# Kernel optimization log

Hardware: AMD Instinct MI355X
Metric: run time of the kernel (lower is better)

## Reference

```python
import jax, jax.numpy as jnp
import numpy as np
import math

B, S, E, H = 2, 4096, 1024, 1024

def setup_inputs() -> dict:
    key = jax.random.key(0)
    ks = jax.random.split(key, 7)
    X = jax.random.normal(ks[0], (B, S, E), dtype=jnp.float32)
    attention_mask = jnp.ones((B, S, S), dtype=jnp.int32)
    sc = 1.0 / math.sqrt(E)
    Wq = jax.random.normal(ks[1], (H, E), dtype=jnp.float32) * sc
    Wk = jax.random.normal(ks[2], (H, E), dtype=jnp.float32) * sc
    Wv = jax.random.normal(ks[3], (H, E), dtype=jnp.float32) * sc
    bq = jnp.zeros((H,), dtype=jnp.float32)
    bk = jnp.zeros((H,), dtype=jnp.float32)
    bv = jnp.zeros((H,), dtype=jnp.float32)
    return {"X": X, "attention_mask": attention_mask,
            "Wq": Wq, "bq": bq, "Wk": Wk, "bk": bk, "Wv": Wv, "bv": bv}

def reference(X, attention_mask, Wq, bq, Wk, bk, Wv, bv):
    # Linear layers: y = x @ W^T + b (torch convention W is [out, in])
    Q = jnp.einsum('bse,he->bsh', X, Wq) + bq
    K = jnp.einsum('bse,he->bsh', X, Wk) + bk
    V = jnp.einsum('bse,he->bsh', X, Wv) + bv
    scale = 1.0 / math.sqrt(H)
    scores = jnp.einsum('bqh,bkh->bqk', Q, K) * scale  # [B,S,S]
    scores = jnp.where(attention_mask == 0, -jnp.inf, scores)
    # dropout (eval mode -> identity) would be applied here, BEFORE softmax
    weights = jax.nn.softmax(scores, axis=-1)
    out = jnp.einsum('bqk,bkh->bqh', weights, V)  # [B,S,H]
    return out
```

## Files before the change

kernel.cpp:

```cpp
#include <hip/hip_runtime.h>
#include <stdint.h>


typedef __bf16 bf16;
typedef __attribute__((ext_vector_type(4))) __bf16 bf16x4;
typedef __attribute__((ext_vector_type(8))) __bf16 bf16x8;
typedef __attribute__((ext_vector_type(4))) float f32x4;

__device__ __forceinline__ void g2l16(const void* g, void* l) {
  __builtin_amdgcn_global_load_lds(
      (const __attribute__((address_space(1))) uint32_t*)g,
      (__attribute__((address_space(3))) uint32_t*)l, 16, 0, 0);
}

__device__ __forceinline__ f32x4 ds_read128(uint32_t addr) {
  f32x4 d;
  asm volatile("ds_read_b128 %0, %1" : "=v"(d) : "v"(addr));
  return d;
}

template <int V> struct IC { static constexpr int value = V; };
template <bool V> struct BC { static constexpr bool value = V; };

template <int N> __device__ __forceinline__ void waitvm() {
  if constexpr (N == 6) asm volatile("s_waitcnt vmcnt(6)" ::: "memory");
  else if constexpr (N == 4) asm volatile("s_waitcnt vmcnt(4)" ::: "memory");
  else if constexpr (N == 0) asm volatile("s_waitcnt vmcnt(0)" ::: "memory");
}

__global__ __launch_bounds__(256) void cvt_all(
    const float* __restrict__ X, const float* __restrict__ Wq,
    const float* __restrict__ Wk, const float* __restrict__ Wv,
    bf16* __restrict__ X_bf, bf16* __restrict__ W_bf) {
  const int bid = blockIdx.x;
  const float* src;
  bf16* dst;
  int i;
  if (bid < 4096) {
    i = (bid * 256 + threadIdx.x) * 8;
    src = X; dst = X_bf;
  } else {
    i = ((bid - 4096) * 256 + threadIdx.x) * 8;
    const int seg = i >> 20;
    const int off = i & 1048575;
    src = (seg == 0) ? Wq : (seg == 1) ? Wk : Wv;
    dst = W_bf;
    f32x4 a = *(const f32x4*)(src + off);
    f32x4 b = *(const f32x4*)(src + off + 4);
    bf16x8 o;
#pragma unroll
    for (int e = 0; e < 4; ++e) { o[e] = (bf16)a[e]; o[4 + e] = (bf16)b[e]; }
    *(bf16x8*)(dst + i) = o;
    return;
  }
  f32x4 a = *(const f32x4*)(src + i);
  f32x4 b = *(const f32x4*)(src + i + 4);
  bf16x8 o;
#pragma unroll
  for (int e = 0; e < 4; ++e) { o[e] = (bf16)a[e]; o[4 + e] = (bf16)b[e]; }
  *(bf16x8*)(dst + i) = o;
}

template <int NT>
__device__ __forceinline__ void kloop256(
    const bf16* __restrict__ Ag, const bf16* __restrict__ Bg, const int KA,
    const int KB, bf16* lds, f32x4 (&acc)[8][4]) {
  const int tid = threadIdx.x;
  const int lane = tid & 63;
  const int wave = tid >> 6;
  const int l15 = lane & 15, quad = lane >> 4;
  const int wrow = (wave >> 2) * 128;
  const int wcol = (wave & 3) * 64;
  const int srow = tid >> 3;
  const int scol = ((tid & 7) ^ (srow & 7)) * 8;
  const int swz = l15 & 7;

  const uint32_t lds_u = (uint32_t)(uintptr_t)lds;
  const uint32_t a_l15 = lds_u + (uint32_t)((wrow + l15) * 128);
  const uint32_t b_l15 = lds_u + 32768u + (uint32_t)((wcol + l15) * 128);
  const uint32_t ck0 = (uint32_t)(((quad) ^ swz) * 16);
  const uint32_t ck1 = (uint32_t)(((4 + quad) ^ swz) * 16);

  auto stg = [&](int t, int h) {
    bf16* base = lds + (t & 1) * 32768;
    if (h == 0) {
      const bf16* g = Bg + (size_t)srow * KB + t * 64 + scol;
      g2l16(g, base + 16384 + tid * 8);
      g2l16(g + (size_t)64 * KB, base + 16384 + tid * 8 + 4096);
    } else if (h == 1) {
      const bf16* g = Bg + (size_t)(128 + srow) * KB + t * 64 + scol;
      g2l16(g, base + 24576 + tid * 8);
      g2l16(g + (size_t)64 * KB, base + 24576 + tid * 8 + 4096);
    } else if (h == 2) {
      const bf16* g = Ag + (size_t)srow * KA + t * 64 + scol;
      g2l16(g, base + tid * 8);
      g2l16(g + (size_t)128 * KA, base + tid * 8 + 8192);
    } else {
      const bf16* g = Ag + (size_t)(64 + srow) * KA + t * 64 + scol;
      g2l16(g, base + 4096 + tid * 8);
      g2l16(g + (size_t)128 * KA, base + 4096 + tid * 8 + 8192);
    }
  };

  f32x4 brf[2][4];
  auto phase = [&](int t, auto qc, int st, int sh, auto dsc, auto vmc) {
    constexpr int q = decltype(qc)::value;
    constexpr bool ds = decltype(dsc)::value;
    constexpr int vm = decltype(vmc)::value;
    const uint32_t bb = (t & 1) ? 65536u : 0u;
    f32x4 ar[2][2];
#pragma unroll
    for (int i = 0; i < 2; ++i) {
      ar[i][0] = ds_read128(a_l15 + bb + (uint32_t)((2 * q + i) * 2048) + ck0);
      ar[i][1] = ds_read128(a_l15 + bb + (uint32_t)((2 * q + i) * 2048) + ck1);
    }
    if constexpr (q == 0) {
#pragma unroll
      for (int j = 0; j < 4; ++j) {
        brf[0][j] = ds_read128(b_l15 + bb + (uint32_t)(j * 2048) + ck0);
        brf[1][j] = ds_read128(b_l15 + bb + (uint32_t)(j * 2048) + ck1);
      }
    }
    if constexpr (ds) stg(st, sh);
    __builtin_amdgcn_s_barrier();
    asm volatile("s_waitcnt lgkmcnt(0)" ::: "memory");
    __builtin_amdgcn_sched_barrier(0);
    __builtin_amdgcn_s_setprio(1);
#pragma unroll
    for (int ks = 0; ks < 2; ++ks)
#pragma unroll
      for (int i = 0; i < 2; ++i)
#pragma unroll
        for (int j = 0; j < 4; ++j)
          acc[2 * q + i][j] = __builtin_amdgcn_mfma_f32_16x16x32_bf16(
              __builtin_bit_cast(bf16x8, ar[i][ks]),
              __builtin_bit_cast(bf16x8, brf[ks][j]),
              acc[2 * q + i][j], 0, 0, 0);
    __builtin_amdgcn_s_setprio(0);
    waitvm<vm>();
    __builtin_amdgcn_s_barrier();
  };

  stg(0, 0); stg(0, 1); stg(0, 2); stg(0, 3);
  stg(1, 0); stg(1, 1); stg(1, 2);
  asm volatile("s_waitcnt vmcnt(6)" ::: "memory");
  __builtin_amdgcn_s_barrier();

  constexpr int NI = NT / 2;
#pragma unroll 1
  for (int u = 0; u < NI - 1; ++u) {
    const int t0 = 2 * u, t1 = t0 + 1;
    phase(t0, IC<0>{}, t1, 3, BC<true>{}, IC<-1>{});
    phase(t0, IC<1>{}, t0 + 2, 0, BC<true>{}, IC<-1>{});
    phase(t0, IC<2>{}, t0 + 2, 1, BC<true>{}, IC<-1>{});
    phase(t0, IC<3>{}, t0 + 2, 2, BC<true>{}, IC<6>{});
    phase(t1, IC<0>{}, t0 + 2, 3, BC<true>{}, IC<-1>{});
    phase(t1, IC<1>{}, t0 + 3, 0, BC<true>{}, IC<-1>{});
    phase(t1, IC<2>{}, t0 + 3, 1, BC<true>{}, IC<-1>{});
    phase(t1, IC<3>{}, t0 + 3, 2, BC<true>{}, IC<6>{});
  }
  {
    const int t0 = NT - 2, t1 = NT - 1;
    phase(t0, IC<0>{}, t1, 3, BC<true>{}, IC<-1>{});
    phase(t0, IC<1>{}, 0, 0, BC<false>{}, IC<-1>{});
    phase(t0, IC<2>{}, 0, 0, BC<false>{}, IC<-1>{});
    phase(t0, IC<3>{}, 0, 0, BC<false>{}, IC<0>{});
    phase(t1, IC<0>{}, 0, 0, BC<false>{}, IC<-1>{});
    phase(t1, IC<1>{}, 0, 0, BC<false>{}, IC<-1>{});
    phase(t1, IC<2>{}, 0, 0, BC<false>{}, IC<-1>{});
    phase(t1, IC<3>{}, 0, 0, BC<false>{}, IC<-1>{});
  }
}

__global__ __launch_bounds__(256, 2) void gemm_qkv(
    const bf16* __restrict__ Xb, const bf16* __restrict__ Wb3,
    const float* __restrict__ bq, const float* __restrict__ bk,
    const float* __restrict__ bv, bf16* __restrict__ QK,
    bf16* __restrict__ Vt)
{
  constexpr int K = 1024, N = 1024;
  __shared__ __align__(16) bf16 ldsA[128 * 64];
  __shared__ __align__(16) bf16 ldsB[128 * 64];

  const int tid  = threadIdx.x;
  const int lane = tid & 63;
  const int wave = tid >> 6;
  const int d = blockIdx.y * 64 + blockIdx.x;
  const int xcd = d & 7, slot = d >> 3;
  const int g = xcd * 8 + slot / 24;
  const int c = slot % 24;
  const int which = c >> 3;
  const int n0 = (c & 7) * 128;
  const int m0 = g * 128;
  const bf16* Bt = Wb3 + (size_t)which * 1048576;
  const float* bias = (which == 0) ? bq : ((which == 1) ? bk : bv);

  const int l15  = lane & 15;
  const int quad = lane >> 4;
  const int wm = (wave >> 1) * 64;
  const int wn = (wave & 1) * 64;
  const int sw = l15 & 7;

  f32x4 acc[4][4];
#pragma unroll
  for (int i = 0; i < 4; ++i)
#pragma unroll
    for (int j = 0; j < 4; ++j) acc[i][j] = f32x4{0.f, 0.f, 0.f, 0.f};

  const int srow = tid >> 3;
  const int scol = ((tid & 7) ^ (srow & 7)) * 8;
  const size_t a_base = (size_t)(m0 + srow) * K + scol;
  const size_t b_base = (size_t)(n0 + srow) * K + scol;
  const int lds_off = tid * 8;

  for (int kt = 0; kt < K; kt += 64) {
    const bf16* ga = Xb + a_base + kt;
    const bf16* gb = Bt + b_base + kt;
#pragma unroll
    for (int it = 0; it < 4; ++it) {
      g2l16(ga + (size_t)(it * 32) * K, &ldsA[lds_off + it * 2048]);
      g2l16(gb + (size_t)(it * 32) * K, &ldsB[lds_off + it * 2048]);
    }
    __syncthreads();
#pragma unroll
    for (int ks = 0; ks < 2; ++ks) {
      const int ch = ks * 4 + quad;
      bf16x8 af[4], bfg[4];
#pragma unroll
      for (int i = 0; i < 4; ++i)
        af[i] = *(const bf16x8*)&ldsA[(wm + i * 16 + l15) * 64 + (ch ^ sw) * 8];
#pragma unroll
      for (int j = 0; j < 4; ++j)
        bfg[j] = *(const bf16x8*)&ldsB[(wn + j * 16 + l15) * 64 + (ch ^ sw) * 8];
#pragma unroll
      for (int i = 0; i < 4; ++i)
#pragma unroll
        for (int j = 0; j < 4; ++j)
          acc[i][j] = __builtin_amdgcn_mfma_f32_16x16x32_bf16(
              af[i], bfg[j], acc[i][j], 0, 0, 0);
    }
    __syncthreads();
  }

  if (which < 2) {
    bf16* C = QK + (size_t)which * (size_t)(8192 * 1024);
#pragma unroll
    for (int i = 0; i < 4; ++i) {
#pragma unroll
      for (int j = 0; j < 4; ++j) {
        const int r = m0 + wm + i * 16 + quad * 4;
        const int cc = n0 + wn + j * 16 + l15;
        const float bvv = bias[cc];
        f32x4 v = acc[i][j];
#pragma unroll
        for (int reg = 0; reg < 4; ++reg)
          C[(size_t)(r + reg) * N + cc] = (bf16)(v[reg] + bvv);
      }
    }
  } else {
#pragma unroll
    for (int i = 0; i < 4; ++i) {
#pragma unroll
      for (int j = 0; j < 4; ++j) {
        const int r = m0 + wm + i * 16 + quad * 4;
        const int cc = n0 + wn + j * 16 + l15;
        const int b = r >> 12, s = r & 4095;
        const float bvv = bias[cc];
        f32x4 v = acc[i][j];
        bf16x4 o;
#pragma unroll
        for (int reg = 0; reg < 4; ++reg) o[reg] = (bf16)(v[reg] + bvv);
        *(bf16x4*)&Vt[((size_t)(b * 1024 + cc)) * 4096 + s] = o;
      }
    }
  }
}

__global__ __launch_bounds__(512, 2) void gemm_scores(
    const bf16* __restrict__ Q, const bf16* __restrict__ Kb,
    const int* __restrict__ mask, bf16* __restrict__ P,
    float* __restrict__ psum) {
  __shared__ __align__(16) bf16 lds[2 * 32768];
  const int bid = blockIdx.y * 32 + blockIdx.x;
  const int sb = (bid & 7) * 64 + (bid >> 3);
  const int bx = sb & 31, by = sb >> 5;
  const int m0 = bx * 256;
  const int n0 = by * 256;
  const int batch = m0 >> 12;
  const bf16* Ag = Q + (size_t)m0 * 1024;
  const bf16* Bg = Kb + (size_t)batch * (size_t)(4096 * 1024) +
                   (size_t)n0 * 1024;

  f32x4 acc[8][4];
#pragma unroll
  for (int i = 0; i < 8; ++i)
#pragma unroll
    for (int j = 0; j < 4; ++j) acc[i][j] = f32x4{0.f, 0.f, 0.f, 0.f};

  kloop256<16>(Ag, Bg, 1024, 1024, lds, acc);

  const int lane = threadIdx.x & 63, wave = threadIdx.x >> 6;
  const int l15 = lane & 15, quad = lane >> 4;
  const int wrow = (wave >> 2) * 128, wcol = (wave & 3) * 64;
  float* ps = psum + (size_t)(by * 4 + (wave & 3)) * 8192;

#pragma unroll
  for (int i = 0; i < 8; ++i) {
    const int r = m0 + wrow + i * 16 + quad * 4;
    f32x4 rsum = f32x4{0.f, 0.f, 0.f, 0.f};
#pragma unroll
    for (int j = 0; j < 4; ++j) {
      const int c = n0 + wcol + j * 16 + l15;
      f32x4 v = acc[i][j];
#pragma unroll
      for (int reg = 0; reg < 4; ++reg) {
        float e = __expf(v[reg] * 0.03125f);
        if (mask[(size_t)(r + reg) * 4096 + c] == 0) e = 0.f;
        P[(size_t)(r + reg) * 4096 + c] = (bf16)e;
        rsum[reg] += e;
      }
    }
#pragma unroll
    for (int off = 1; off < 16; off <<= 1) {
#pragma unroll
      for (int reg = 0; reg < 4; ++reg)
        rsum[reg] += __shfl_xor(rsum[reg], off);
    }
    if (l15 == 0) {
#pragma unroll
      for (int reg = 0; reg < 4; ++reg) ps[r + reg] = rsum[reg];
    }
  }
}

__global__ __launch_bounds__(256, 2) void gemm_pv(
    const bf16* __restrict__ A, const bf16* __restrict__ Bt,
    const float* __restrict__ psum, float* __restrict__ C)
{
  constexpr int N = 1024, K = 4096;
  __shared__ __align__(16) bf16 ldsA[128 * 64];
  __shared__ __align__(16) bf16 ldsB[128 * 64];

  const int tid  = threadIdx.x;
  const int lane = tid & 63;
  const int wave = tid >> 6;
  const int d = blockIdx.y * 64 + blockIdx.x;
  const int xcd = d & 7, slot = d >> 3;
  const int g = xcd * 8 + (slot >> 3);
  const int h = slot & 7;
  const int m0 = g * 128;
  const int n0 = h * 128;
  const int batch = m0 >> 12;
  const bf16* Btb = Bt + (size_t)batch * (size_t)(1024 * 4096);

  const int l15  = lane & 15;
  const int quad = lane >> 4;
  const int wm = (wave >> 1) * 64;
  const int wn = (wave & 1) * 64;
  const int sw = l15 & 7;

  f32x4 acc[4][4];
#pragma unroll
  for (int i = 0; i < 4; ++i)
#pragma unroll
    for (int j = 0; j < 4; ++j) acc[i][j] = f32x4{0.f, 0.f, 0.f, 0.f};

  const int srow = tid >> 3;
  const int scol = ((tid & 7) ^ (srow & 7)) * 8;
  const size_t a_base = (size_t)(m0 + srow) * K + scol;
  const size_t b_base = (size_t)(n0 + srow) * K + scol;
  const int lds_off = tid * 8;

  for (int kt = 0; kt < K; kt += 64) {
    const bf16* ga = A + a_base + kt;
    const bf16* gb = Btb + b_base + kt;
#pragma unroll
    for (int it = 0; it < 4; ++it) {
      g2l16(ga + (size_t)(it * 32) * K, &ldsA[lds_off + it * 2048]);
      g2l16(gb + (size_t)(it * 32) * K, &ldsB[lds_off + it * 2048]);
    }
    __syncthreads();
#pragma unroll
    for (int ks = 0; ks < 2; ++ks) {
      const int ch = ks * 4 + quad;
      bf16x8 af[4], bfg[4];
#pragma unroll
      for (int i = 0; i < 4; ++i)
        af[i] = *(const bf16x8*)&ldsA[(wm + i * 16 + l15) * 64 + (ch ^ sw) * 8];
#pragma unroll
      for (int j = 0; j < 4; ++j)
        bfg[j] = *(const bf16x8*)&ldsB[(wn + j * 16 + l15) * 64 + (ch ^ sw) * 8];
#pragma unroll
      for (int i = 0; i < 4; ++i)
#pragma unroll
        for (int j = 0; j < 4; ++j)
          acc[i][j] = __builtin_amdgcn_mfma_f32_16x16x32_bf16(
              af[i], bfg[j], acc[i][j], 0, 0, 0);
    }
    __syncthreads();
  }

  float* linv = (float*)ldsA;
  if (tid < 128) {
    float s = 0.f;
#pragma unroll 8
    for (int p = 0; p < 64; ++p) s += psum[(size_t)p * 8192 + m0 + tid];
    linv[tid] = 1.0f / s;
  }
  __syncthreads();

#pragma unroll
  for (int i = 0; i < 4; ++i) {
    const int lr = wm + i * 16 + quad * 4;
    const int r = m0 + lr;
    f32x4 inv;
#pragma unroll
    for (int reg = 0; reg < 4; ++reg) inv[reg] = linv[lr + reg];
#pragma unroll
    for (int j = 0; j < 4; ++j) {
      const int c = n0 + wn + j * 16 + l15;
      f32x4 v = acc[i][j];
#pragma unroll
      for (int reg = 0; reg < 4; ++reg)
        C[(size_t)(r + reg) * N + c] = v[reg] * inv[reg];
    }
  }
}

extern "C" void kernel_launch(void* const* d_in, const int* in_sizes, int n_in,
                              void* d_out, int out_size, void* d_ws,
                              size_t ws_size, hipStream_t stream) {
  const float* X   = (const float*)d_in[0];
  const int* mask  = (const int*)d_in[1];
  const float* Wq  = (const float*)d_in[2];
  const float* bq  = (const float*)d_in[3];
  const float* Wk  = (const float*)d_in[4];
  const float* bk  = (const float*)d_in[5];
  const float* Wv  = (const float*)d_in[6];
  const float* bv  = (const float*)d_in[7];
  float* out = (float*)d_out;

  const size_t QKV_ELEMS = (size_t)8192 * 1024;
  bf16* Q    = (bf16*)d_ws;
  bf16* Kb   = Q + QKV_ELEMS;
  bf16* X_bf = Kb + QKV_ELEMS;
  bf16* Vt   = X_bf + QKV_ELEMS;
  bf16* Sc   = Vt + QKV_ELEMS;
  bf16* W_bf = Sc;
  float* psum = (float*)X_bf;

  cvt_all<<<dim3(5632), dim3(256), 0, stream>>>(X, Wq, Wk, Wv, X_bf, W_bf);
  gemm_qkv<<<dim3(64, 24), dim3(256), 0, stream>>>(X_bf, W_bf, bq, bk, bv, Q,
                                                   Vt);
  gemm_scores<<<dim3(32, 16), dim3(512), 0, stream>>>(Q, Kb, mask, Sc, psum);
  gemm_pv<<<dim3(64, 8), dim3(256), 0, stream>>>(Sc, Vt, psum, out);
}
```

Before: 414.6 us.

## Switch all GEMM kernels from 16x16x32 to 32x32x16 MFMA tiles

Replaces the 16x16x32 bf16 MFMA instruction with 32x32x16 across the QKV projection, QK^T/softmax and PV kernels. Fragment loading, LDS addressing, accumulator layout and epilogue index mapping are reworked for the 32x32 output layout. The larger MFMA tile needs fewer LDS reads per FLOP and fewer instructions, which should lift matrix-core throughput. In exchange the epilogue stores are more scattered, and the row-sum reduction needs wider shuffles over 16 registers each.

```diff
diff --git a/kernel.cpp b/kernel.cpp
--- a/kernel.cpp
+++ b/kernel.cpp
@@ -6,6 +6,7 @@
 typedef __attribute__((ext_vector_type(4))) __bf16 bf16x4;
 typedef __attribute__((ext_vector_type(8))) __bf16 bf16x8;
 typedef __attribute__((ext_vector_type(4))) float f32x4;
+typedef __attribute__((ext_vector_type(16))) float f32x16;
 
 __device__ __forceinline__ void g2l16(const void* g, void* l) {
   __builtin_amdgcn_global_load_lds(
@@ -64,22 +65,24 @@
 template <int NT>
 __device__ __forceinline__ void kloop256(
     const bf16* __restrict__ Ag, const bf16* __restrict__ Bg, const int KA,
-    const int KB, bf16* lds, f32x4 (&acc)[8][4]) {
+    const int KB, bf16* lds, f32x16 (&acc)[4][2]) {
   const int tid = threadIdx.x;
   const int lane = tid & 63;
   const int wave = tid >> 6;
-  const int l15 = lane & 15, quad = lane >> 4;
+  const int l31 = lane & 31, hi = lane >> 5;
   const int wrow = (wave >> 2) * 128;
   const int wcol = (wave & 3) * 64;
   const int srow = tid >> 3;
   const int scol = ((tid & 7) ^ (srow & 7)) * 8;
-  const int swz = l15 & 7;
+  const int swz = l31 & 7;
 
   const uint32_t lds_u = (uint32_t)(uintptr_t)lds;
-  const uint32_t a_l15 = lds_u + (uint32_t)((wrow + l15) * 128);
-  const uint32_t b_l15 = lds_u + 32768u + (uint32_t)((wcol + l15) * 128);
-  const uint32_t ck0 = (uint32_t)(((quad) ^ swz) * 16);
-  const uint32_t ck1 = (uint32_t)(((4 + quad) ^ swz) * 16);
+  const uint32_t a_l = lds_u + (uint32_t)((wrow + l31) * 128);
+  const uint32_t b_l = lds_u + 32768u + (uint32_t)((wcol + l31) * 128);
+  uint32_t ckk[4];
+#pragma unroll
+  for (int ks = 0; ks < 4; ++ks)
+    ckk[ks] = (uint32_t)(((ks * 2 + hi) ^ swz) * 16);
 
   auto stg = [&](int t, int h) {
     bf16* base = lds + (t & 1) * 32768;
@@ -108,18 +111,16 @@
     constexpr bool ds = decltype(dsc)::value;
     constexpr int vm = decltype(vmc)::value;
     const uint32_t bb = (t & 1) ? 65536u : 0u;
-    f32x4 ar[2][2];
-#pragma unroll
-    for (int i = 0; i < 2; ++i) {
-      ar[i][0] = ds_read128(a_l15 + bb + (uint32_t)((2 * q + i) * 2048) + ck0);
-      ar[i][1] = ds_read128(a_l15 + bb + (uint32_t)((2 * q + i) * 2048) + ck1);
-    }
+    f32x4 ar[4];
+#pragma unroll
+    for (int ks = 0; ks < 4; ++ks)
+      ar[ks] = ds_read128(a_l + bb + (uint32_t)(q * 4096) + ckk[ks]);
     if constexpr (q == 0) {
 #pragma unroll
-      for (int j = 0; j < 4; ++j) {
-        brf[0][j] = ds_read128(b_l15 + bb + (uint32_t)(j * 2048) + ck0);
-        brf[1][j] = ds_read128(b_l15 + bb + (uint32_t)(j * 2048) + ck1);
-      }
+      for (int nj = 0; nj < 2; ++nj)
+#pragma unroll
+        for (int ks = 0; ks < 4; ++ks)
+          brf[nj][ks] = ds_read128(b_l + bb + (uint32_t)(nj * 4096) + ckk[ks]);
     }
     if constexpr (ds) stg(st, sh);
     __builtin_amdgcn_s_barrier();
@@ -127,15 +128,13 @@
     __builtin_amdgcn_sched_barrier(0);
     __builtin_amdgcn_s_setprio(1);
 #pragma unroll
-    for (int ks = 0; ks < 2; ++ks)
-#pragma unroll
-      for (int i = 0; i < 2; ++i)
-#pragma unroll
-        for (int j = 0; j < 4; ++j)
-          acc[2 * q + i][j] = __builtin_amdgcn_mfma_f32_16x16x32_bf16(
-              __builtin_bit_cast(bf16x8, ar[i][ks]),
-              __builtin_bit_cast(bf16x8, brf[ks][j]),
-              acc[2 * q + i][j], 0, 0, 0);
+    for (int ks = 0; ks < 4; ++ks)
+#pragma unroll
+      for (int nj = 0; nj < 2; ++nj)
+        acc[q][nj] = __builtin_amdgcn_mfma_f32_32x32x16_bf16(
+            __builtin_bit_cast(bf16x8, ar[ks]),
+            __builtin_bit_cast(bf16x8, brf[nj][ks]),
+            acc[q][nj], 0, 0, 0);
     __builtin_amdgcn_s_setprio(0);
     waitvm<vm>();
     __builtin_amdgcn_s_barrier();
@@ -188,24 +187,23 @@
   const int d = blockIdx.y * 64 + blockIdx.x;
   const int xcd = d & 7, slot = d >> 3;
   const int g = xcd * 8 + slot / 24;
-  const int c = slot % 24;
-  const int which = c >> 3;
-  const int n0 = (c & 7) * 128;
+  const int c3 = slot % 24;
+  const int which = c3 >> 3;
+  const int n0 = (c3 & 7) * 128;
   const int m0 = g * 128;
   const bf16* Bt = Wb3 + (size_t)which * 1048576;
   const float* bias = (which == 0) ? bq : ((which == 1) ? bk : bv);
 
-  const int l15  = lane & 15;
-  const int quad = lane >> 4;
+  const int l31 = lane & 31, hi = lane >> 5;
   const int wm = (wave >> 1) * 64;
   const int wn = (wave & 1) * 64;
-  const int sw = l15 & 7;
-
-  f32x4 acc[4][4];
-#pragma unroll
-  for (int i = 0; i < 4; ++i)
-#pragma unroll
-    for (int j = 0; j < 4; ++j) acc[i][j] = f32x4{0.f, 0.f, 0.f, 0.f};
+  const int sw = l31 & 7;
+
+  f32x16 acc[2][2];
+#pragma unroll
+  for (int i = 0; i < 2; ++i)
+#pragma unroll
+    for (int j = 0; j < 2; ++j) acc[i][j] = (f32x16)(0.f);
 
   const int srow = tid >> 3;
   const int scol = ((tid & 7) ^ (srow & 7)) * 8;
@@ -223,21 +221,21 @@
     }
     __syncthreads();
 #pragma unroll
-    for (int ks = 0; ks < 2; ++ks) {
-      const int ch = ks * 4 + quad;
-      bf16x8 af[4], bfg[4];
-#pragma unroll
-      for (int i = 0; i < 4; ++i)
-        af[i] = *(const bf16x8*)&ldsA[(wm + i * 16 + l15) * 64 + (ch ^ sw) * 8];
-#pragma unroll
-      for (int j = 0; j < 4; ++j)
-        bfg[j] = *(const bf16x8*)&ldsB[(wn + j * 16 + l15) * 64 + (ch ^ sw) * 8];
-#pragma unroll
-      for (int i = 0; i < 4; ++i)
-#pragma unroll
-        for (int j = 0; j < 4; ++j)
-          acc[i][j] = __builtin_amdgcn_mfma_f32_16x16x32_bf16(
-              af[i], bfg[j], acc[i][j], 0, 0, 0);
+    for (int ks = 0; ks < 4; ++ks) {
+      const int ch = (ks * 2 + hi) ^ sw;
+      bf16x8 af[2], bfg[2];
+#pragma unroll
+      for (int mi = 0; mi < 2; ++mi)
+        af[mi] = *(const bf16x8*)&ldsA[(wm + mi * 32 + l31) * 64 + ch * 8];
+#pragma unroll
+      for (int nj = 0; nj < 2; ++nj)
+        bfg[nj] = *(const bf16x8*)&ldsB[(wn + nj * 32 + l31) * 64 + ch * 8];
+#pragma unroll
+      for (int mi = 0; mi < 2; ++mi)
+#pragma unroll
+        for (int nj = 0; nj < 2; ++nj)
+          acc[mi][nj] = __builtin_amdgcn_mfma_f32_32x32x16_bf16(
+              af[mi], bfg[nj], acc[mi][nj], 0, 0, 0);
     }
     __syncthreads();
   }
@@ -245,32 +243,37 @@
   if (which < 2) {
     bf16* C = QK + (size_t)which * (size_t)(8192 * 1024);
 #pragma unroll
-    for (int i = 0; i < 4; ++i) {
-#pragma unroll
-      for (int j = 0; j < 4; ++j) {
-        const int r = m0 + wm + i * 16 + quad * 4;
-        const int cc = n0 + wn + j * 16 + l15;
+    for (int mi = 0; mi < 2; ++mi) {
+      const int rb = m0 + wm + mi * 32 + 4 * hi;
+#pragma unroll
+      for (int nj = 0; nj < 2; ++nj) {
+        const int cc = n0 + wn + nj * 32 + l31;
         const float bvv = bias[cc];
-        f32x4 v = acc[i][j];
-#pragma unroll
-        for (int reg = 0; reg < 4; ++reg)
-          C[(size_t)(r + reg) * N + cc] = (bf16)(v[reg] + bvv);
+#pragma unroll
+        for (int gq = 0; gq < 4; ++gq)
+#pragma unroll
+          for (int k = 0; k < 4; ++k)
+            C[(size_t)(rb + 8 * gq + k) * N + cc] =
+                (bf16)(acc[mi][nj][4 * gq + k] + bvv);
       }
     }
   } else {
 #pragma unroll
-    for (int i = 0; i < 4; ++i) {
-#pragma unroll
-      for (int j = 0; j < 4; ++j) {
-        const int r = m0 + wm + i * 16 + quad * 4;
-        const int cc = n0 + wn + j * 16 + l15;
-        const int b = r >> 12, s = r & 4095;
+    for (int mi = 0; mi < 2; ++mi) {
+      const int rb = m0 + wm + mi * 32 + 4 * hi;
+#pragma unroll
+      for (int nj = 0; nj < 2; ++nj) {
+        const int cc = n0 + wn + nj * 32 + l31;
         const float bvv = bias[cc];
-        f32x4 v = acc[i][j];
-        bf16x4 o;
-#pragma unroll
-        for (int reg = 0; reg < 4; ++reg) o[reg] = (bf16)(v[reg] + bvv);
-        *(bf16x4*)&Vt[((size_t)(b * 1024 + cc)) * 4096 + s] = o;
+#pragma unroll
+        for (int gq = 0; gq < 4; ++gq) {
+          const int r0 = rb + 8 * gq;
+          const int b = r0 >> 12, s = r0 & 4095;
+          bf16x4 o;
+#pragma unroll
+          for (int k = 0; k < 4; ++k) o[k] = (bf16)(acc[mi][nj][4 * gq + k] + bvv);
+          *(bf16x4*)&Vt[((size_t)(b * 1024 + cc)) * 4096 + s] = o;
+        }
       }
     }
   }
@@ -291,44 +294,47 @@
   const bf16* Bg = Kb + (size_t)batch * (size_t)(4096 * 1024) +
                    (size_t)n0 * 1024;
 
-  f32x4 acc[8][4];
-#pragma unroll
-  for (int i = 0; i < 8; ++i)
-#pragma unroll
-    for (int j = 0; j < 4; ++j) acc[i][j] = f32x4{0.f, 0.f, 0.f, 0.f};
+  f32x16 acc[4][2];
+#pragma unroll
+  for (int i = 0; i < 4; ++i)
+#pragma unroll
+    for (int j = 0; j < 2; ++j) acc[i][j] = (f32x16)(0.f);
 
   kloop256<16>(Ag, Bg, 1024, 1024, lds, acc);
 
   const int lane = threadIdx.x & 63, wave = threadIdx.x >> 6;
-  const int l15 = lane & 15, quad = lane >> 4;
+  const int l31 = lane & 31, hi = lane >> 5;
   const int wrow = (wave >> 2) * 128, wcol = (wave & 3) * 64;
   float* ps = psum + (size_t)(by * 4 + (wave & 3)) * 8192;
 
 #pragma unroll
-  for (int i = 0; i < 8; ++i) {
-    const int r = m0 + wrow + i * 16 + quad * 4;
-    f32x4 rsum = f32x4{0.f, 0.f, 0.f, 0.f};
-#pragma unroll
-    for (int j = 0; j < 4; ++j) {
-      const int c = n0 + wcol + j * 16 + l15;
-      f32x4 v = acc[i][j];
-#pragma unroll
-      for (int reg = 0; reg < 4; ++reg) {
-        float e = __expf(v[reg] * 0.03125f);
-        if (mask[(size_t)(r + reg) * 4096 + c] == 0) e = 0.f;
-        P[(size_t)(r + reg) * 4096 + c] = (bf16)e;
+  for (int mi = 0; mi < 4; ++mi) {
+    const int rb = m0 + wrow + mi * 32 + 4 * hi;
+    float rsum[16];
+#pragma unroll
+    for (int reg = 0; reg < 16; ++reg) rsum[reg] = 0.f;
+#pragma unroll
+    for (int nj = 0; nj < 2; ++nj) {
+      const int c = n0 + wcol + nj * 32 + l31;
+#pragma unroll
+      for (int reg = 0; reg < 16; ++reg) {
+        const int r = rb + (reg & 3) + 8 * (reg >> 2);
+        float e = __expf(acc[mi][nj][reg] * 0.03125f);
+        if (mask[(size_t)r * 4096 + c] == 0) e = 0.f;
+        P[(size_t)r * 4096 + c] = (bf16)e;
         rsum[reg] += e;
       }
     }
 #pragma unroll
-    for (int off = 1; off < 16; off <<= 1) {
-#pragma unroll
-      for (int reg = 0; reg < 4; ++reg)
+    for (int off = 1; off < 32; off <<= 1) {
+#pragma unroll
+      for (int reg = 0; reg < 16; ++reg)
         rsum[reg] += __shfl_xor(rsum[reg], off);
     }
-    if (l15 == 0) {
-#pragma unroll
-      for (int reg = 0; reg < 4; ++reg) ps[r + reg] = rsum[reg];
+    if (l31 == 0) {
+#pragma unroll
+      for (int reg = 0; reg < 16; ++reg)
+        ps[rb + (reg & 3) + 8 * (reg >> 2)] = rsum[reg];
     }
   }
 }
@@ -353,17 +359,16 @@
   const int batch = m0 >> 12;
   const bf16* Btb = Bt + (size_t)batch * (size_t)(1024 * 4096);
 
-  const int l15  = lane & 15;
-  const int quad = lane >> 4;
+  const int l31 = lane & 31, hi = lane >> 5;
   const int wm = (wave >> 1) * 64;
   const int wn = (wave & 1) * 64;
-  const int sw = l15 & 7;
-
-  f32x4 acc[4][4];
-#pragma unroll
-  for (int i = 0; i < 4; ++i)
-#pragma unroll
-    for (int j = 0; j < 4; ++j) acc[i][j] = f32x4{0.f, 0.f, 0.f, 0.f};
+  const int sw = l31 & 7;
+
+  f32x16 acc[2][2];
+#pragma unroll
+  for (int i = 0; i < 2; ++i)
+#pragma unroll
+    for (int j = 0; j < 2; ++j) acc[i][j] = (f32x16)(0.f);
 
   const int srow = tid >> 3;
   const int scol = ((tid & 7) ^ (srow & 7)) * 8;
@@ -381,21 +386,21 @@
     }
     __syncthreads();
 #pragma unroll
-    for (int ks = 0; ks < 2; ++ks) {
-      const int ch = ks * 4 + quad;
-      bf16x8 af[4], bfg[4];
-#pragma unroll
-      for (int i = 0; i < 4; ++i)
-        af[i] = *(const bf16x8*)&ldsA[(wm + i * 16 + l15) * 64 + (ch ^ sw) * 8];
-#pragma unroll
-      for (int j = 0; j < 4; ++j)
-        bfg[j] = *(const bf16x8*)&ldsB[(wn + j * 16 + l15) * 64 + (ch ^ sw) * 8];
-#pragma unroll
-      for (int i = 0; i < 4; ++i)
-#pragma unroll
-        for (int j = 0; j < 4; ++j)
-          acc[i][j] = __builtin_amdgcn_mfma_f32_16x16x32_bf16(
-              af[i], bfg[j], acc[i][j], 0, 0, 0);
+    for (int ks = 0; ks < 4; ++ks) {
+      const int ch = (ks * 2 + hi) ^ sw;
+      bf16x8 af[2], bfg[2];
+#pragma unroll
+      for (int mi = 0; mi < 2; ++mi)
+        af[mi] = *(const bf16x8*)&ldsA[(wm + mi * 32 + l31) * 64 + ch * 8];
+#pragma unroll
+      for (int nj = 0; nj < 2; ++nj)
+        bfg[nj] = *(const bf16x8*)&ldsB[(wn + nj * 32 + l31) * 64 + ch * 8];
+#pragma unroll
+      for (int mi = 0; mi < 2; ++mi)
+#pragma unroll
+        for (int nj = 0; nj < 2; ++nj)
+          acc[mi][nj] = __builtin_amdgcn_mfma_f32_32x32x16_bf16(
+              af[mi], bfg[nj], acc[mi][nj], 0, 0, 0);
     }
     __syncthreads();
   }
@@ -410,19 +415,18 @@
   __syncthreads();
 
 #pragma unroll
-  for (int i = 0; i < 4; ++i) {
-    const int lr = wm + i * 16 + quad * 4;
-    const int r = m0 + lr;
-    f32x4 inv;
-#pragma unroll
-    for (int reg = 0; reg < 4; ++reg) inv[reg] = linv[lr + reg];
-#pragma unroll
-    for (int j = 0; j < 4; ++j) {
-      const int c = n0 + wn + j * 16 + l15;
-      f32x4 v = acc[i][j];
-#pragma unroll
-      for (int reg = 0; reg < 4; ++reg)
-        C[(size_t)(r + reg) * N + c] = v[reg] * inv[reg];
+  for (int mi = 0; mi < 2; ++mi) {
+    const int lrb = wm + mi * 32 + 4 * hi;
+#pragma unroll
+    for (int nj = 0; nj < 2; ++nj) {
+      const int c = n0 + wn + nj * 32 + l31;
+#pragma unroll
+      for (int gq = 0; gq < 4; ++gq)
+#pragma unroll
+        for (int k = 0; k < 4; ++k) {
+          const int lr = lrb + 8 * gq + k;
+          C[(size_t)(m0 + lr) * N + c] = acc[mi][nj][4 * gq + k] * linv[lr];
+        }
     }
   }
 }
```

Result: slower. 457.4 us (+10.3%).
